# Kernel optimization log

Hardware: AMD Instinct MI355X
Metric: run time of the kernel (lower is better)

The kernel has to match this reference:

```python
import jax, jax.numpy as jnp
import numpy as np

N_HEAD = 16
ROPE_THETA = 10000.0


def _rope_cache(T, dim, theta=ROPE_THETA):
    # inv_freq over even indices, as in RotaryEmbedding
    inv_freq = 1.0 / (theta ** (jnp.arange(0, dim, 2, dtype=jnp.float32) / dim))
    freqs = jnp.arange(T, dtype=jnp.float32)[:, None] * inv_freq[None, :]  # [T, dim//2]
    return jnp.cos(freqs), jnp.sin(freqs)


def _apply_rope(x, cos, sin):
    # x: [B, H, T, D]; cos/sin: [T, D//2] broadcast over B,H
    x1 = x[..., ::2]
    x2 = x[..., 1::2]
    # even slots: x1*cos - x2*sin ; odd slots: x2*cos + x1*sin (interleaved rotate-pairs)
    r1 = x1 * cos - x2 * sin
    r2 = x2 * cos + x1 * sin
    return jnp.stack([r1, r2], axis=-1).reshape(x.shape)


def setup_inputs() -> dict:
    key = jax.random.key(0)
    k1, k2, k3 = jax.random.split(key, 3)
    B, T, C = 4, 2048, 1024
    x = jax.random.normal(k1, (B, T, C), dtype=jnp.float32)
    W_qkv = jax.random.normal(k2, (C, 3 * C), dtype=jnp.float32) * (C ** -0.5)
    W_out = jax.random.normal(k3, (C, C), dtype=jnp.float32) * (C ** -0.5)
    return {"x": x, "W_qkv": W_qkv, "W_out": W_out}


def reference(x, W_qkv, W_out):
    B, T, C = x.shape
    H = N_HEAD
    D = C // H
    # fused QKV projection -> [3, B, H, T, D]
    qkv = (x @ W_qkv).reshape(B, T, 3, H, D).transpose(2, 0, 3, 1, 4)
    q, k, v = qkv[0], qkv[1], qkv[2]
    cos, sin = _rope_cache(T, D)
    q = _apply_rope(q, cos, sin)
    k = _apply_rope(k, cos, sin)
    scale = 1.0 / jnp.sqrt(jnp.float32(D))
    scores = jnp.einsum('bhqd,bhkd->bhqk', q, k) * scale  # [B,H,T,T]
    causal_mask = jnp.tril(jnp.ones((T, T), dtype=bool))
    scores = jnp.where(causal_mask, scores, -jnp.inf)
    attn = jax.nn.softmax(scores, axis=-1)
    out = jnp.einsum('bhqk,bhkd->bhqd', attn, v)  # [B,H,T,D]
    out = out.transpose(0, 2, 1, 3).reshape(B, T, C)
    return out @ W_out
```

## Files before the change

kernel.cpp:

```cpp
#include <hip/hip_runtime.h>
#include <hip/hip_bf16.h>
#include <math.h>

#define BATCH 4
#define SEQ   2048
#define CDIM  1024
#define NHEAD 16
#define HDIM  64
#define QKVN  3072
#define QSCALE 0.1803368801111244f

typedef float f32x4 __attribute__((ext_vector_type(4)));
typedef short bf16x8 __attribute__((ext_vector_type(8)));
typedef short bf16x4 __attribute__((ext_vector_type(4)));

static __device__ __forceinline__ unsigned short f2bf(float f) {
    unsigned int u = __float_as_uint(f);
    u += 0x7FFF + ((u >> 16) & 1);
    return (unsigned short)(u >> 16);
}
static __device__ __forceinline__ float bf2f(unsigned short u) {
    return __uint_as_float(((unsigned int)u) << 16);
}
static __device__ __forceinline__ unsigned int pk2bf(float lo, float hi) {
    __hip_bfloat162 h = __float22bfloat162_rn(make_float2(lo, hi));
    return *(unsigned int*)&h;
}
static __device__ __forceinline__ bf16x8 lds_read8(const unsigned short* p) {
    bf16x4 lo = *(const bf16x4*)p;
    bf16x4 hi = *(const bf16x4*)(p + 4);
    return __builtin_shufflevector(lo, hi, 0, 1, 2, 3, 4, 5, 6, 7);
}

__global__ __launch_bounds__(256) void convert_bf16(const float* __restrict__ src,
                                                    unsigned short* __restrict__ dst,
                                                    int n4) {
    int i = blockIdx.x * 256 + threadIdx.x;
    if (i >= n4) return;
    float4 v = ((const float4*)src)[i];
    ushort4 o;
    o.x = f2bf(v.x); o.y = f2bf(v.y); o.z = f2bf(v.z); o.w = f2bf(v.w);
    ((ushort4*)dst)[i] = o;
}

__global__ __launch_bounds__(256) void transpose_bf16(const float* __restrict__ W,
                                                      unsigned short* __restrict__ Wt,
                                                      int K, int N) {
    __shared__ unsigned short tile[64][65];
    const int tid = threadIdx.x;
    const int n0 = blockIdx.x * 64;
    const int k0 = blockIdx.y * 64;
    const int r = tid >> 4;
    const int c4 = (tid & 15) << 2;
    #pragma unroll
    for (int ii = 0; ii < 4; ii++) {
        int row = r + 16 * ii;
        float4 v = *(const float4*)&W[(size_t)(k0 + row) * N + n0 + c4];
        tile[c4 + 0][row] = f2bf(v.x);
        tile[c4 + 1][row] = f2bf(v.y);
        tile[c4 + 2][row] = f2bf(v.z);
        tile[c4 + 3][row] = f2bf(v.w);
    }
    __syncthreads();
    #pragma unroll
    for (int ii = 0; ii < 4; ii++) {
        int row = r + 16 * ii;
        ushort4 o;
        o.x = tile[row][c4 + 0];
        o.y = tile[row][c4 + 1];
        o.z = tile[row][c4 + 2];
        o.w = tile[row][c4 + 3];
        *(ushort4*)&Wt[(size_t)(n0 + row) * K + k0 + c4] = o;
    }
}

#define GLDS(gp, lp) __builtin_amdgcn_global_load_lds(                       \
    (const __attribute__((address_space(1))) unsigned int*)(gp),             \
    (__attribute__((address_space(3))) unsigned int*)(lp), 16, 0, 0)

template <typename OUT>
__global__ __launch_bounds__(256) void gemm_bt_bf16(
    const unsigned short* __restrict__ A,
    const unsigned short* __restrict__ Bt,
    OUT* __restrict__ C, int M, int N, int K) {
    __shared__ unsigned short As[128 * 32];
    __shared__ unsigned short Bs[128 * 32];

    const int tid = threadIdx.x;
    const int wave = tid >> 6;
    const int lane = tid & 63;
    const int bm = blockIdx.y * 128;
    const int bn = blockIdx.x * 128;
    const int wm = (wave >> 1) * 64;
    const int wn = (wave & 1) * 64;

    const int srow = tid >> 2;
    const int scol = (((tid & 3) ^ ((tid >> 3) & 3)) << 3);
    const unsigned short* Ag0 = A + (size_t)(bm + srow) * K + scol;
    const unsigned short* Ag1 = A + (size_t)(bm + 64 + srow) * K + scol;
    const unsigned short* Bg0 = Bt + (size_t)(bn + srow) * K + scol;
    const unsigned short* Bg1 = Bt + (size_t)(bn + 64 + srow) * K + scol;
    char* AsW = (char*)As + wave * 1024;
    char* BsW = (char*)Bs + wave * 1024;

    const int fm = lane & 15;
    const int quad = lane >> 4;
    const int ck = (quad ^ ((fm >> 1) & 3)) << 3;

    f32x4 acc[4][4];
    #pragma unroll
    for (int i = 0; i < 4; i++)
        #pragma unroll
        for (int j = 0; j < 4; j++)
            acc[i][j] = (f32x4){0.f, 0.f, 0.f, 0.f};

    for (int k0 = 0; k0 < K; k0 += 32) {
        GLDS(Ag0 + k0, AsW);
        GLDS(Ag1 + k0, AsW + 4096);
        GLDS(Bg0 + k0, BsW);
        GLDS(Bg1 + k0, BsW + 4096);
        __syncthreads();

        bf16x8 af[4], bfr[4];
        #pragma unroll
        for (int i = 0; i < 4; i++)
            af[i] = *(const bf16x8*)&As[(wm + i * 16 + fm) * 32 + ck];
        #pragma unroll
        for (int j = 0; j < 4; j++)
            bfr[j] = *(const bf16x8*)&Bs[(wn + j * 16 + fm) * 32 + ck];
        #pragma unroll
        for (int i = 0; i < 4; i++)
            #pragma unroll
            for (int j = 0; j < 4; j++)
                acc[i][j] = __builtin_amdgcn_mfma_f32_16x16x32_bf16(
                    af[i], bfr[j], acc[i][j], 0, 0, 0);
        __syncthreads();
    }

    const int er = quad * 4;
    #pragma unroll
    for (int i = 0; i < 4; i++) {
        #pragma unroll
        for (int j = 0; j < 4; j++) {
            #pragma unroll
            for (int r = 0; r < 4; r++) {
                size_t off = (size_t)(bm + wm + i * 16 + er + r) * N + bn + wn + j * 16 + fm;
                if constexpr (sizeof(OUT) == 2)
                    C[off] = f2bf(acc[i][j][r]);
                else
                    C[off] = acc[i][j][r];
            }
        }
    }
}

__global__ __launch_bounds__(256) void rope_qk(const unsigned short* __restrict__ qkvb,
                                               unsigned short* __restrict__ Qg,
                                               unsigned short* __restrict__ Kg) {
    const int i = blockIdx.x * 256 + threadIdx.x;
    const int c4 = (i & 15) << 2;
    const int h = (i >> 4) & 15;
    const int s = (i >> 8) & 1;
    const int t = (i >> 9) & 2047;
    const int b = i >> 20;

    ushort4 v = *(const ushort4*)&qkvb[(((size_t)(b * SEQ + t) * 3 + s) * CDIM) + h * HDIM + c4];
    float x0 = bf2f(v.x), x1 = bf2f(v.y), x2 = bf2f(v.z), x3 = bf2f(v.w);
    const float invf0 = powf(10000.0f, -((float)c4) / 64.0f);
    const float invf1 = powf(10000.0f, -((float)(c4 + 2)) / 64.0f);
    float s0, c0, s1, c1;
    __sincosf((float)t * invf0, &s0, &c0);
    __sincosf((float)t * invf1, &s1, &c1);
    const float sc = s == 0 ? QSCALE : 1.0f;
    ushort4 o;
    o.x = f2bf((x0 * c0 - x1 * s0) * sc);
    o.y = f2bf((x1 * c0 + x0 * s0) * sc);
    o.z = f2bf((x2 * c1 - x3 * s1) * sc);
    o.w = f2bf((x3 * c1 + x2 * s1) * sc);
    unsigned short* dst = (s == 0) ? Qg : Kg;
    *(ushort4*)&dst[((size_t)(b * NHEAD + h) * SEQ + t) * HDIM + c4] = o;
}

__global__ __launch_bounds__(256) void transpose_v(const unsigned short* __restrict__ qkvb,
                                                   unsigned short* __restrict__ Vtg) {
    __shared__ unsigned short tile[64 * 68];
    const int tid = threadIdx.x;
    const int tt = blockIdx.x;
    const int bh = blockIdx.y;
    const int b = bh >> 4, h = bh & 15;
    const int r = tid >> 4;
    const int c4 = (tid & 15) << 2;
    #pragma unroll
    for (int ii = 0; ii < 4; ii++) {
        int row = r + 16 * ii;
        ushort4 v = *(const ushort4*)&qkvb[(((size_t)(b * SEQ + tt * 64 + row) * 3 + 2) * CDIM) + h * HDIM + c4];
        *(ushort4*)&tile[row * 68 + c4] = v;
    }
    __syncthreads();
    #pragma unroll
    for (int ii = 0; ii < 4; ii++) {
        int d = r + 16 * ii;
        ushort4 o;
        o.x = tile[(c4 + 0) * 68 + d];
        o.y = tile[(c4 + 1) * 68 + d];
        o.z = tile[(c4 + 2) * 68 + d];
        o.w = tile[(c4 + 3) * 68 + d];
        *(ushort4*)&Vtg[((size_t)bh * HDIM + d) * SEQ + tt * 64 + c4] = o;
    }
}

__global__ __launch_bounds__(256, 4) void flash_attn_mfma(
    const unsigned short* __restrict__ Qg,
    const unsigned short* __restrict__ Kg,
    const unsigned short* __restrict__ Vtg,
    unsigned short* __restrict__ att) {
    __shared__ unsigned short Ks[64 * 68];
    __shared__ unsigned short Vt[64 * 68];
    __shared__ unsigned short Ps[128 * 68];

    const int tid = threadIdx.x;
    const int wave = tid >> 6;
    const int lane = tid & 63;
    const int fm = lane & 15;
    const int quad = lane >> 4;
    const int fq = quad << 3;
    const int wq = wave * 32;
    const int bh = blockIdx.x & 63;
    const int qt = 15 - (blockIdx.x >> 6);
    const int b = bh >> 4, h = bh & 15;

    const int r_ld = tid >> 4;
    const int c4 = (tid & 15) << 2;

    bf16x8 aq[2][2];
    #pragma unroll
    for (int i = 0; i < 2; i++)
        #pragma unroll
        for (int ks = 0; ks < 2; ks++)
            aq[i][ks] = *(const bf16x8*)&Qg[((size_t)bh * SEQ + qt * 128 + wq + i * 16 + fm) * HDIM + ks * 32 + fq];

    bf16x8 bones;
    #pragma unroll
    for (int z = 0; z < 8; z++) bones[z] = (short)0x3F80;

    f32x4 O[2][4], lsum[2];
    #pragma unroll
    for (int i = 0; i < 2; i++) {
        lsum[i] = (f32x4){0.f, 0.f, 0.f, 0.f};
        #pragma unroll
        for (int dt = 0; dt < 4; dt++) O[i][dt] = (f32x4){0.f, 0.f, 0.f, 0.f};
    }

    const int jtop = 2 * qt + 1;
    for (int j = 0; j <= jtop; j++) {
        #pragma unroll
        for (int ii = 0; ii < 4; ii++) {
            const int row = r_ld + 16 * ii;
            *(ushort4*)&Ks[row * 68 + c4] =
                *(const ushort4*)&Kg[((size_t)bh * SEQ + j * 64 + row) * HDIM + c4];
            *(ushort4*)&Vt[row * 68 + c4] =
                *(const ushort4*)&Vtg[((size_t)bh * HDIM + row) * SEQ + j * 64 + c4];
        }
        __syncthreads();

        const bool active = (j * 64) <= (qt * 128 + wq + 31);
        if (active) {
            f32x4 sa[2][4];
            #pragma unroll
            for (int i = 0; i < 2; i++)
                #pragma unroll
                for (int jj = 0; jj < 4; jj++)
                    sa[i][jj] = (f32x4){0.f, 0.f, 0.f, 0.f};
            #pragma unroll
            for (int ks = 0; ks < 2; ks++) {
                #pragma unroll
                for (int jj = 0; jj < 4; jj++) {
                    bf16x8 bk = lds_read8(&Ks[(jj * 16 + fm) * 68 + ks * 32 + fq]);
                    sa[0][jj] = __builtin_amdgcn_mfma_f32_16x16x32_bf16(aq[0][ks], bk, sa[0][jj], 0, 0, 0);
                    sa[1][jj] = __builtin_amdgcn_mfma_f32_16x16x32_bf16(aq[1][ks], bk, sa[1][jj], 0, 0, 0);
                }
            }

            if (j * 64 + 63 > qt * 128 + wq) {
                const int kb = j * 64 + fm;
                #pragma unroll
                for (int i = 0; i < 2; i++) {
                    const int rb = qt * 128 + wq + i * 16 + quad * 4;
                    #pragma unroll
                    for (int jj = 0; jj < 4; jj++)
                        #pragma unroll
                        for (int r = 0; r < 4; r++)
                            if (kb + jj * 16 > rb + r) sa[i][jj][r] = -INFINITY;
                }
            }

            #pragma unroll
            for (int i = 0; i < 2; i++) {
                const int prow = (wq + i * 16 + quad * 4) * 68 + fm;
                #pragma unroll
                for (int jj = 0; jj < 4; jj++) {
                    const float e0 = exp2f(sa[i][jj][0]);
                    const float e1 = exp2f(sa[i][jj][1]);
                    const float e2 = exp2f(sa[i][jj][2]);
                    const float e3 = exp2f(sa[i][jj][3]);
                    const unsigned int p01 = pk2bf(e0, e1);
                    const unsigned int p23 = pk2bf(e2, e3);
                    Ps[prow + 0 * 68 + jj * 16] = (unsigned short)p01;
                    Ps[prow + 1 * 68 + jj * 16] = (unsigned short)(p01 >> 16);
                    Ps[prow + 2 * 68 + jj * 16] = (unsigned short)p23;
                    Ps[prow + 3 * 68 + jj * 16] = (unsigned short)(p23 >> 16);
                }
            }

            #pragma unroll
            for (int ks = 0; ks < 2; ks++) {
                bf16x8 ap0 = lds_read8(&Ps[(wq + fm) * 68 + ks * 32 + fq]);
                bf16x8 ap1 = lds_read8(&Ps[(wq + 16 + fm) * 68 + ks * 32 + fq]);
                lsum[0] = __builtin_amdgcn_mfma_f32_16x16x32_bf16(ap0, bones, lsum[0], 0, 0, 0);
                lsum[1] = __builtin_amdgcn_mfma_f32_16x16x32_bf16(ap1, bones, lsum[1], 0, 0, 0);
                #pragma unroll
                for (int dt = 0; dt < 4; dt++) {
                    bf16x8 bv = lds_read8(&Vt[(dt * 16 + fm) * 68 + ks * 32 + fq]);
                    O[0][dt] = __builtin_amdgcn_mfma_f32_16x16x32_bf16(ap0, bv, O[0][dt], 0, 0, 0);
                    O[1][dt] = __builtin_amdgcn_mfma_f32_16x16x32_bf16(ap1, bv, O[1][dt], 0, 0, 0);
                }
            }
        }
        __syncthreads();
    }

    #pragma unroll
    for (int i = 0; i < 2; i++) {
        #pragma unroll
        for (int r = 0; r < 4; r++) {
            const float inv_l = 1.0f / lsum[i][r];
            const int row = qt * 128 + wq + i * 16 + quad * 4 + r;
            #pragma unroll
            for (int dt = 0; dt < 4; dt++)
                att[(size_t)(b * SEQ + row) * CDIM + h * HDIM + dt * 16 + fm] =
                    f2bf(O[i][dt][r] * inv_l);
        }
    }
}

extern "C" void kernel_launch(void* const* d_in, const int* in_sizes, int n_in,
                              void* d_out, int out_size, void* d_ws, size_t ws_size,
                              hipStream_t stream) {
    const float* x     = (const float*)d_in[0];
    const float* W_qkv = (const float*)d_in[1];
    const float* W_out = (const float*)d_in[2];
    float* out = (float*)d_out;

    const int M = BATCH * SEQ;

    unsigned short* qkvb = (unsigned short*)d_ws;
    unsigned short* xb   = qkvb + (size_t)M * QKVN;
    unsigned short* wqb  = xb + (size_t)M * CDIM;
    unsigned short* wob  = wqb + (size_t)CDIM * QKVN;
    unsigned short* attb = wob + (size_t)CDIM * CDIM;
    unsigned short* Qg   = attb + (size_t)M * CDIM;
    unsigned short* Kg   = Qg + (size_t)M * CDIM;
    unsigned short* Vtg  = Kg + (size_t)M * CDIM;

    convert_bf16<<<(M * CDIM / 4 + 255) / 256, 256, 0, stream>>>(x, xb, M * CDIM / 4);
    transpose_bf16<<<dim3(QKVN / 64, CDIM / 64), 256, 0, stream>>>(W_qkv, wqb, CDIM, QKVN);
    transpose_bf16<<<dim3(CDIM / 64, CDIM / 64), 256, 0, stream>>>(W_out, wob, CDIM, CDIM);

    gemm_bt_bf16<unsigned short><<<dim3(QKVN / 128, M / 128), 256, 0, stream>>>(
        xb, wqb, qkvb, M, QKVN, CDIM);

    rope_qk<<<(BATCH * SEQ * 2 * NHEAD * 16) / 256, 256, 0, stream>>>(qkvb, Qg, Kg);
    transpose_v<<<dim3(SEQ / 64, BATCH * NHEAD), 256, 0, stream>>>(qkvb, Vtg);

    flash_attn_mfma<<<BATCH * NHEAD * (SEQ / 128), 256, 0, stream>>>(Qg, Kg, Vtg, attb);

    gemm_bt_bf16<float><<<dim3(CDIM / 128, M / 128), 256, 0, stream>>>(
        attb, wob, out, M, CDIM, CDIM);
}
```

Baseline: 305.0 us.

## Shrink flash-attention query tile to 64 rows and raise occupancy

The attention kernel now handles 64 query rows per block, with each wave owning 16 rows instead of 32. This doubles the grid, drops the per-wave active-mask branch because the diagonal block is always the last one, halves the P scratch tile and register use, and raises the launch-bounds occupancy hint from 4 to 6. The aim is finer causal load balancing and more blocks resident per CU. The cost is that each K/V tile loaded to shared memory now serves half as many query rows, so global/LDS traffic per unit of work rises.

```diff
diff --git a/kernel.cpp b/kernel.cpp
--- a/kernel.cpp
+++ b/kernel.cpp
@@ -209,14 +209,14 @@
     }
 }
 
-__global__ __launch_bounds__(256, 4) void flash_attn_mfma(
+__global__ __launch_bounds__(256, 6) void flash_attn_mfma(
     const unsigned short* __restrict__ Qg,
     const unsigned short* __restrict__ Kg,
     const unsigned short* __restrict__ Vtg,
     unsigned short* __restrict__ att) {
     __shared__ unsigned short Ks[64 * 68];
     __shared__ unsigned short Vt[64 * 68];
-    __shared__ unsigned short Ps[128 * 68];
+    __shared__ unsigned short Ps[64 * 68];
 
     const int tid = threadIdx.x;
     const int wave = tid >> 6;
@@ -224,35 +224,29 @@
     const int fm = lane & 15;
     const int quad = lane >> 4;
     const int fq = quad << 3;
-    const int wq = wave * 32;
+    const int wq = wave * 16;
     const int bh = blockIdx.x & 63;
-    const int qt = 15 - (blockIdx.x >> 6);
+    const int qt = 31 - (blockIdx.x >> 6);
     const int b = bh >> 4, h = bh & 15;
 
     const int r_ld = tid >> 4;
     const int c4 = (tid & 15) << 2;
 
-    bf16x8 aq[2][2];
-    #pragma unroll
-    for (int i = 0; i < 2; i++)
-        #pragma unroll
-        for (int ks = 0; ks < 2; ks++)
-            aq[i][ks] = *(const bf16x8*)&Qg[((size_t)bh * SEQ + qt * 128 + wq + i * 16 + fm) * HDIM + ks * 32 + fq];
+    bf16x8 aq[2];
+    #pragma unroll
+    for (int ks = 0; ks < 2; ks++)
+        aq[ks] = *(const bf16x8*)&Qg[((size_t)bh * SEQ + qt * 64 + wq + fm) * HDIM + ks * 32 + fq];
 
     bf16x8 bones;
     #pragma unroll
     for (int z = 0; z < 8; z++) bones[z] = (short)0x3F80;
 
-    f32x4 O[2][4], lsum[2];
-    #pragma unroll
-    for (int i = 0; i < 2; i++) {
-        lsum[i] = (f32x4){0.f, 0.f, 0.f, 0.f};
-        #pragma unroll
-        for (int dt = 0; dt < 4; dt++) O[i][dt] = (f32x4){0.f, 0.f, 0.f, 0.f};
-    }
-
-    const int jtop = 2 * qt + 1;
-    for (int j = 0; j <= jtop; j++) {
+    f32x4 O[4], lsum;
+    lsum = (f32x4){0.f, 0.f, 0.f, 0.f};
+    #pragma unroll
+    for (int dt = 0; dt < 4; dt++) O[dt] = (f32x4){0.f, 0.f, 0.f, 0.f};
+
+    for (int j = 0; j <= qt; j++) {
         #pragma unroll
         for (int ii = 0; ii < 4; ii++) {
             const int row = r_ld + 16 * ii;
@@ -263,83 +257,67 @@
         }
         __syncthreads();
 
-        const bool active = (j * 64) <= (qt * 128 + wq + 31);
-        if (active) {
-            f32x4 sa[2][4];
-            #pragma unroll
-            for (int i = 0; i < 2; i++)
+        f32x4 sa[4];
+        #pragma unroll
+        for (int jj = 0; jj < 4; jj++)
+            sa[jj] = (f32x4){0.f, 0.f, 0.f, 0.f};
+        #pragma unroll
+        for (int ks = 0; ks < 2; ks++) {
+            #pragma unroll
+            for (int jj = 0; jj < 4; jj++) {
+                bf16x8 bk = lds_read8(&Ks[(jj * 16 + fm) * 68 + ks * 32 + fq]);
+                sa[jj] = __builtin_amdgcn_mfma_f32_16x16x32_bf16(aq[ks], bk, sa[jj], 0, 0, 0);
+            }
+        }
+
+        if (j == qt) {
+            const int kb = j * 64 + fm;
+            const int rb = qt * 64 + wq + quad * 4;
+            #pragma unroll
+            for (int jj = 0; jj < 4; jj++)
                 #pragma unroll
-                for (int jj = 0; jj < 4; jj++)
-                    sa[i][jj] = (f32x4){0.f, 0.f, 0.f, 0.f};
-            #pragma unroll
-            for (int ks = 0; ks < 2; ks++) {
-                #pragma unroll
-                for (int jj = 0; jj < 4; jj++) {
-                    bf16x8 bk = lds_read8(&Ks[(jj * 16 + fm) * 68 + ks * 32 + fq]);
-                    sa[0][jj] = __builtin_amdgcn_mfma_f32_16x16x32_bf16(aq[0][ks], bk, sa[0][jj], 0, 0, 0);
-                    sa[1][jj] = __builtin_amdgcn_mfma_f32_16x16x32_bf16(aq[1][ks], bk, sa[1][jj], 0, 0, 0);
-                }
+                for (int r = 0; r < 4; r++)
+                    if (kb + jj * 16 > rb + r) sa[jj][r] = -INFINITY;
+        }
+
+        {
+            const int prow = (wq + quad * 4) * 68 + fm;
+            #pragma unroll
+            for (int jj = 0; jj < 4; jj++) {
+                const float e0 = exp2f(sa[jj][0]);
+                const float e1 = exp2f(sa[jj][1]);
+                const float e2 = exp2f(sa[jj][2]);
+                const float e3 = exp2f(sa[jj][3]);
+                const unsigned int p01 = pk2bf(e0, e1);
+                const unsigned int p23 = pk2bf(e2, e3);
+                Ps[prow + 0 * 68 + jj * 16] = (unsigned short)p01;
+                Ps[prow + 1 * 68 + jj * 16] = (unsigned short)(p01 >> 16);
+                Ps[prow + 2 * 68 + jj * 16] = (unsigned short)p23;
+                Ps[prow + 3 * 68 + jj * 16] = (unsigned short)(p23 >> 16);
             }
-
-            if (j * 64 + 63 > qt * 128 + wq) {
-                const int kb = j * 64 + fm;
-                #pragma unroll
-                for (int i = 0; i < 2; i++) {
-                    const int rb = qt * 128 + wq + i * 16 + quad * 4;
-                    #pragma unroll
-                    for (int jj = 0; jj < 4; jj++)
-                        #pragma unroll
-                        for (int r = 0; r < 4; r++)
-                            if (kb + jj * 16 > rb + r) sa[i][jj][r] = -INFINITY;
-                }
+        }
+
+        #pragma unroll
+        for (int ks = 0; ks < 2; ks++) {
+            bf16x8 ap = lds_read8(&Ps[(wq + fm) * 68 + ks * 32 + fq]);
+            lsum = __builtin_amdgcn_mfma_f32_16x16x32_bf16(ap, bones, lsum, 0, 0, 0);
+            #pragma unroll
+            for (int dt = 0; dt < 4; dt++) {
+                bf16x8 bv = lds_read8(&Vt[(dt * 16 + fm) * 68 + ks * 32 + fq]);
+                O[dt] = __builtin_amdgcn_mfma_f32_16x16x32_bf16(ap, bv, O[dt], 0, 0, 0);
             }
-
-            #pragma unroll
-            for (int i = 0; i < 2; i++) {
-                const int prow = (wq + i * 16 + quad * 4) * 68 + fm;
-                #pragma unroll
-                for (int jj = 0; jj < 4; jj++) {
-                    const float e0 = exp2f(sa[i][jj][0]);
-                    const float e1 = exp2f(sa[i][jj][1]);
-                    const float e2 = exp2f(sa[i][jj][2]);
-                    const float e3 = exp2f(sa[i][jj][3]);
-                    const unsigned int p01 = pk2bf(e0, e1);
-                    const unsigned int p23 = pk2bf(e2, e3);
-                    Ps[prow + 0 * 68 + jj * 16] = (unsigned short)p01;
-                    Ps[prow + 1 * 68 + jj * 16] = (unsigned short)(p01 >> 16);
-                    Ps[prow + 2 * 68 + jj * 16] = (unsigned short)p23;
-                    Ps[prow + 3 * 68 + jj * 16] = (unsigned short)(p23 >> 16);
-                }
-            }
-
-            #pragma unroll
-            for (int ks = 0; ks < 2; ks++) {
-                bf16x8 ap0 = lds_read8(&Ps[(wq + fm) * 68 + ks * 32 + fq]);
-                bf16x8 ap1 = lds_read8(&Ps[(wq + 16 + fm) * 68 + ks * 32 + fq]);
-                lsum[0] = __builtin_amdgcn_mfma_f32_16x16x32_bf16(ap0, bones, lsum[0], 0, 0, 0);
-                lsum[1] = __builtin_amdgcn_mfma_f32_16x16x32_bf16(ap1, bones, lsum[1], 0, 0, 0);
-                #pragma unroll
-                for (int dt = 0; dt < 4; dt++) {
-                    bf16x8 bv = lds_read8(&Vt[(dt * 16 + fm) * 68 + ks * 32 + fq]);
-                    O[0][dt] = __builtin_amdgcn_mfma_f32_16x16x32_bf16(ap0, bv, O[0][dt], 0, 0, 0);
-                    O[1][dt] = __builtin_amdgcn_mfma_f32_16x16x32_bf16(ap1, bv, O[1][dt], 0, 0, 0);
-                }
-            }
         }
         __syncthreads();
     }
 
     #pragma unroll
-    for (int i = 0; i < 2; i++) {
-        #pragma unroll
-        for (int r = 0; r < 4; r++) {
-            const float inv_l = 1.0f / lsum[i][r];
-            const int row = qt * 128 + wq + i * 16 + quad * 4 + r;
-            #pragma unroll
-            for (int dt = 0; dt < 4; dt++)
-                att[(size_t)(b * SEQ + row) * CDIM + h * HDIM + dt * 16 + fm] =
-                    f2bf(O[i][dt][r] * inv_l);
-        }
+    for (int r = 0; r < 4; r++) {
+        const float inv_l = 1.0f / lsum[r];
+        const int row = qt * 64 + wq + quad * 4 + r;
+        #pragma unroll
+        for (int dt = 0; dt < 4; dt++)
+            att[(size_t)(b * SEQ + row) * CDIM + h * HDIM + dt * 16 + fm] =
+                f2bf(O[dt][r] * inv_l);
     }
 }
 
@@ -372,7 +350,7 @@
     rope_qk<<<(BATCH * SEQ * 2 * NHEAD * 16) / 256, 256, 0, stream>>>(qkvb, Qg, Kg);
     transpose_v<<<dim3(SEQ / 64, BATCH * NHEAD), 256, 0, stream>>>(qkvb, Vtg);
 
-    flash_attn_mfma<<<BATCH * NHEAD * (SEQ / 128), 256, 0, stream>>>(Qg, Kg, Vtg, attb);
+    flash_attn_mfma<<<BATCH * NHEAD * (SEQ / 64), 256, 0, stream>>>(Qg, Kg, Vtg, attb);
 
     gemm_bt_bf16<float><<<dim3(CDIM / 128, M / 128), 256, 0, stream>>>(
         attb, wob, out, M, CDIM, CDIM);
```

Result: slower. 336.3 us (+10.3%).

## Pair causal query tiles per block and double-buffer K/V loads in attention

Applied to the files above, without the earlier changes.

Each attention block now handles two query tiles (s and 15-s) one after the other, which balances causal work across 512 blocks instead of 1024 blocks of uneven length. K/V tiles are double-buffered in LDS, and the next tile is prefetched into registers while the current one is computed, so there is one barrier per iteration. The cost is more LDS per block and more registers, and launch bounds drop to 2 blocks per CU, which lowers occupancy.

```diff
diff --git a/kernel.cpp b/kernel.cpp
--- a/kernel.cpp
+++ b/kernel.cpp
@@ -209,13 +209,13 @@
     }
 }
 
-__global__ __launch_bounds__(256, 4) void flash_attn_mfma(
+__global__ __launch_bounds__(256, 2) void flash_attn_mfma(
     const unsigned short* __restrict__ Qg,
     const unsigned short* __restrict__ Kg,
     const unsigned short* __restrict__ Vtg,
     unsigned short* __restrict__ att) {
-    __shared__ unsigned short Ks[64 * 68];
-    __shared__ unsigned short Vt[64 * 68];
+    __shared__ unsigned short Ks[2][64 * 68];
+    __shared__ unsigned short Vt[2][64 * 68];
     __shared__ unsigned short Ps[128 * 68];
 
     const int tid = threadIdx.x;
@@ -225,120 +225,161 @@
     const int quad = lane >> 4;
     const int fq = quad << 3;
     const int wq = wave * 32;
-    const int bh = blockIdx.x & 63;
-    const int qt = 15 - (blockIdx.x >> 6);
+    const int blk = blockIdx.x;
+    const int bh = blk & 63;
+    const int p = blk >> 6;
     const int b = bh >> 4, h = bh & 15;
 
     const int r_ld = tid >> 4;
     const int c4 = (tid & 15) << 2;
 
-    bf16x8 aq[2][2];
-    #pragma unroll
-    for (int i = 0; i < 2; i++)
-        #pragma unroll
-        for (int ks = 0; ks < 2; ks++)
-            aq[i][ks] = *(const bf16x8*)&Qg[((size_t)bh * SEQ + qt * 128 + wq + i * 16 + fm) * HDIM + ks * 32 + fq];
-
     bf16x8 bones;
     #pragma unroll
     for (int z = 0; z < 8; z++) bones[z] = (short)0x3F80;
 
-    f32x4 O[2][4], lsum[2];
-    #pragma unroll
-    for (int i = 0; i < 2; i++) {
-        lsum[i] = (f32x4){0.f, 0.f, 0.f, 0.f};
-        #pragma unroll
-        for (int dt = 0; dt < 4; dt++) O[i][dt] = (f32x4){0.f, 0.f, 0.f, 0.f};
-    }
-
-    const int jtop = 2 * qt + 1;
-    for (int j = 0; j <= jtop; j++) {
+    const unsigned short* Kbase = Kg + (size_t)bh * SEQ * HDIM;
+    const unsigned short* Vbase = Vtg + (size_t)bh * HDIM * SEQ;
+
+    #pragma unroll 1
+    for (int ph = 0; ph < 2; ph++) {
+        const int s = ph ? (15 - p) : p;
+
+        bf16x8 aq[2][2];
+        #pragma unroll
+        for (int i = 0; i < 2; i++)
+            #pragma unroll
+            for (int ks = 0; ks < 2; ks++)
+                aq[i][ks] = *(const bf16x8*)&Qg[((size_t)bh * SEQ + s * 128 + wq + i * 16 + fm) * HDIM + ks * 32 + fq];
+
+        f32x4 O[2][4], lsum[2];
+        #pragma unroll
+        for (int i = 0; i < 2; i++) {
+            lsum[i] = (f32x4){0.f, 0.f, 0.f, 0.f};
+            #pragma unroll
+            for (int dt = 0; dt < 4; dt++) O[i][dt] = (f32x4){0.f, 0.f, 0.f, 0.f};
+        }
+
+        const int jmax = 2 * s + 1;
+
+        ushort4 kreg[4], vreg[4];
         #pragma unroll
         for (int ii = 0; ii < 4; ii++) {
             const int row = r_ld + 16 * ii;
-            *(ushort4*)&Ks[row * 68 + c4] =
-                *(const ushort4*)&Kg[((size_t)bh * SEQ + j * 64 + row) * HDIM + c4];
-            *(ushort4*)&Vt[row * 68 + c4] =
-                *(const ushort4*)&Vtg[((size_t)bh * HDIM + row) * SEQ + j * 64 + c4];
+            kreg[ii] = *(const ushort4*)&Kbase[(size_t)row * HDIM + c4];
+            vreg[ii] = *(const ushort4*)&Vbase[(size_t)row * SEQ + c4];
+        }
+        #pragma unroll
+        for (int ii = 0; ii < 4; ii++) {
+            const int row = r_ld + 16 * ii;
+            *(ushort4*)&Ks[0][row * 68 + c4] = kreg[ii];
+            *(ushort4*)&Vt[0][row * 68 + c4] = vreg[ii];
         }
         __syncthreads();
 
-        const bool active = (j * 64) <= (qt * 128 + wq + 31);
-        if (active) {
-            f32x4 sa[2][4];
-            #pragma unroll
-            for (int i = 0; i < 2; i++)
-                #pragma unroll
-                for (int jj = 0; jj < 4; jj++)
-                    sa[i][jj] = (f32x4){0.f, 0.f, 0.f, 0.f};
-            #pragma unroll
-            for (int ks = 0; ks < 2; ks++) {
-                #pragma unroll
-                for (int jj = 0; jj < 4; jj++) {
-                    bf16x8 bk = lds_read8(&Ks[(jj * 16 + fm) * 68 + ks * 32 + fq]);
-                    sa[0][jj] = __builtin_amdgcn_mfma_f32_16x16x32_bf16(aq[0][ks], bk, sa[0][jj], 0, 0, 0);
-                    sa[1][jj] = __builtin_amdgcn_mfma_f32_16x16x32_bf16(aq[1][ks], bk, sa[1][jj], 0, 0, 0);
+        int cur = 0;
+        #pragma unroll 1
+        for (int j = 0; j <= jmax; j++) {
+            if (j < jmax) {
+                #pragma unroll
+                for (int ii = 0; ii < 4; ii++) {
+                    const int row = r_ld + 16 * ii;
+                    kreg[ii] = *(const ushort4*)&Kbase[(size_t)((j + 1) * 64 + row) * HDIM + c4];
+                    vreg[ii] = *(const ushort4*)&Vbase[(size_t)row * SEQ + (j + 1) * 64 + c4];
                 }
             }
 
-            if (j * 64 + 63 > qt * 128 + wq) {
-                const int kb = j * 64 + fm;
-                #pragma unroll
-                for (int i = 0; i < 2; i++) {
-                    const int rb = qt * 128 + wq + i * 16 + quad * 4;
+            const bool active = (j * 64) <= (s * 128 + wq + 31);
+            if (active) {
+                const unsigned short* Kc = Ks[cur];
+                const unsigned short* Vc = Vt[cur];
+
+                f32x4 sa[2][4];
+                #pragma unroll
+                for (int i = 0; i < 2; i++)
                     #pragma unroll
                     for (int jj = 0; jj < 4; jj++)
+                        sa[i][jj] = (f32x4){0.f, 0.f, 0.f, 0.f};
+                #pragma unroll
+                for (int ks = 0; ks < 2; ks++) {
+                    #pragma unroll
+                    for (int jj = 0; jj < 4; jj++) {
+                        bf16x8 bk = lds_read8(&Kc[(jj * 16 + fm) * 68 + ks * 32 + fq]);
+                        sa[0][jj] = __builtin_amdgcn_mfma_f32_16x16x32_bf16(aq[0][ks], bk, sa[0][jj], 0, 0, 0);
+                        sa[1][jj] = __builtin_amdgcn_mfma_f32_16x16x32_bf16(aq[1][ks], bk, sa[1][jj], 0, 0, 0);
+                    }
+                }
+
+                if (j * 64 + 63 > s * 128 + wq) {
+                    const int kb = j * 64 + fm;
+                    #pragma unroll
+                    for (int i = 0; i < 2; i++) {
+                        const int rb = s * 128 + wq + i * 16 + quad * 4;
                         #pragma unroll
-                        for (int r = 0; r < 4; r++)
-                            if (kb + jj * 16 > rb + r) sa[i][jj][r] = -INFINITY;
+                        for (int jj = 0; jj < 4; jj++)
+                            #pragma unroll
+                            for (int r = 0; r < 4; r++)
+                                if (kb + jj * 16 > rb + r) sa[i][jj][r] = -INFINITY;
+                    }
+                }
+
+                #pragma unroll
+                for (int i = 0; i < 2; i++) {
+                    const int prow = (wq + i * 16 + quad * 4) * 68 + fm;
+                    #pragma unroll
+                    for (int jj = 0; jj < 4; jj++) {
+                        const float e0 = exp2f(sa[i][jj][0]);
+                        const float e1 = exp2f(sa[i][jj][1]);
+                        const float e2 = exp2f(sa[i][jj][2]);
+                        const float e3 = exp2f(sa[i][jj][3]);
+                        const unsigned int p01 = pk2bf(e0, e1);
+                        const unsigned int p23 = pk2bf(e2, e3);
+                        Ps[prow + 0 * 68 + jj * 16] = (unsigned short)p01;
+                        Ps[prow + 1 * 68 + jj * 16] = (unsigned short)(p01 >> 16);
+                        Ps[prow + 2 * 68 + jj * 16] = (unsigned short)p23;
+                        Ps[prow + 3 * 68 + jj * 16] = (unsigned short)(p23 >> 16);
+                    }
+                }
+
+                #pragma unroll
+                for (int ks = 0; ks < 2; ks++) {
+                    bf16x8 ap0 = lds_read8(&Ps[(wq + fm) * 68 + ks * 32 + fq]);
+                    bf16x8 ap1 = lds_read8(&Ps[(wq + 16 + fm) * 68 + ks * 32 + fq]);
+                    lsum[0] = __builtin_amdgcn_mfma_f32_16x16x32_bf16(ap0, bones, lsum[0], 0, 0, 0);
+                    lsum[1] = __builtin_amdgcn_mfma_f32_16x16x32_bf16(ap1, bones, lsum[1], 0, 0, 0);
+                    #pragma unroll
+                    for (int dt = 0; dt < 4; dt++) {
+                        bf16x8 bv = lds_read8(&Vc[(dt * 16 + fm) * 68 + ks * 32 + fq]);
+                        O[0][dt] = __builtin_amdgcn_mfma_f32_16x16x32_bf16(ap0, bv, O[0][dt], 0, 0, 0);
+                        O[1][dt] = __builtin_amdgcn_mfma_f32_16x16x32_bf16(ap1, bv, O[1][dt], 0, 0, 0);
+                    }
                 }
             }
 
+            if (j < jmax) {
+                const int nb = cur ^ 1;
+                #pragma unroll
+                for (int ii = 0; ii < 4; ii++) {
+                    const int row = r_ld + 16 * ii;
+                    *(ushort4*)&Ks[nb][row * 68 + c4] = kreg[ii];
+                    *(ushort4*)&Vt[nb][row * 68 + c4] = vreg[ii];
+                }
+            }
+
+            __syncthreads();
+            cur ^= 1;
+        }
+
+        #pragma unroll
+        for (int i = 0; i < 2; i++) {
             #pragma unroll
-            for (int i = 0; i < 2; i++) {
-                const int prow = (wq + i * 16 + quad * 4) * 68 + fm;
-                #pragma unroll
-                for (int jj = 0; jj < 4; jj++) {
-                    const float e0 = exp2f(sa[i][jj][0]);
-                    const float e1 = exp2f(sa[i][jj][1]);
-                    const float e2 = exp2f(sa[i][jj][2]);
-                    const float e3 = exp2f(sa[i][jj][3]);
-                    const unsigned int p01 = pk2bf(e0, e1);
-                    const unsigned int p23 = pk2bf(e2, e3);
-                    Ps[prow + 0 * 68 + jj * 16] = (unsigned short)p01;
-                    Ps[prow + 1 * 68 + jj * 16] = (unsigned short)(p01 >> 16);
-                    Ps[prow + 2 * 68 + jj * 16] = (unsigned short)p23;
-                    Ps[prow + 3 * 68 + jj * 16] = (unsigned short)(p23 >> 16);
-                }
+            for (int r = 0; r < 4; r++) {
+                const float inv_l = 1.0f / lsum[i][r];
+                const int row = s * 128 + wq + i * 16 + quad * 4 + r;
+                #pragma unroll
+                for (int dt = 0; dt < 4; dt++)
+                    att[(size_t)(b * SEQ + row) * CDIM + h * HDIM + dt * 16 + fm] =
+                        f2bf(O[i][dt][r] * inv_l);
             }
-
-            #pragma unroll
-            for (int ks = 0; ks < 2; ks++) {
-                bf16x8 ap0 = lds_read8(&Ps[(wq + fm) * 68 + ks * 32 + fq]);
-                bf16x8 ap1 = lds_read8(&Ps[(wq + 16 + fm) * 68 + ks * 32 + fq]);
-                lsum[0] = __builtin_amdgcn_mfma_f32_16x16x32_bf16(ap0, bones, lsum[0], 0, 0, 0);
-                lsum[1] = __builtin_amdgcn_mfma_f32_16x16x32_bf16(ap1, bones, lsum[1], 0, 0, 0);
-                #pragma unroll
-                for (int dt = 0; dt < 4; dt++) {
-                    bf16x8 bv = lds_read8(&Vt[(dt * 16 + fm) * 68 + ks * 32 + fq]);
-                    O[0][dt] = __builtin_amdgcn_mfma_f32_16x16x32_bf16(ap0, bv, O[0][dt], 0, 0, 0);
-                    O[1][dt] = __builtin_amdgcn_mfma_f32_16x16x32_bf16(ap1, bv, O[1][dt], 0, 0, 0);
-                }
-            }
-        }
-        __syncthreads();
-    }
-
-    #pragma unroll
-    for (int i = 0; i < 2; i++) {
-        #pragma unroll
-        for (int r = 0; r < 4; r++) {
-            const float inv_l = 1.0f / lsum[i][r];
-            const int row = qt * 128 + wq + i * 16 + quad * 4 + r;
-            #pragma unroll
-            for (int dt = 0; dt < 4; dt++)
-                att[(size_t)(b * SEQ + row) * CDIM + h * HDIM + dt * 16 + fm] =
-                    f2bf(O[i][dt][r] * inv_l);
         }
     }
 }
@@ -372,7 +413,7 @@
     rope_qk<<<(BATCH * SEQ * 2 * NHEAD * 16) / 256, 256, 0, stream>>>(qkvb, Qg, Kg);
     transpose_v<<<dim3(SEQ / 64, BATCH * NHEAD), 256, 0, stream>>>(qkvb, Vtg);
 
-    flash_attn_mfma<<<BATCH * NHEAD * (SEQ / 128), 256, 0, stream>>>(Qg, Kg, Vtg, attb);
+    flash_attn_mfma<<<512, 256, 0, stream>>>(Qg, Kg, Vtg, attb);
 
     gemm_bt_bf16<float><<<dim3(CDIM / 128, M / 128), 256, 0, stream>>>(
         attb, wob, out, M, CDIM, CDIM);
```

New measurement: 312.6 us. 2.5% more time.

## Prefetch next K/V tile into registers during attention compute, add MFMA priority

Applied to the files above, without the earlier changes.

The attention loop now issues global loads for the next K and V tiles into registers before computing on the current tile. After a barrier it writes them into shared memory, so global memory latency overlaps with the MFMA and softmax work. It also raises wave priority around the MFMA blocks with s_setprio. The cost is extra register pressure from the staged tiles, plus a second barrier per iteration.

```diff
diff --git a/kernel.cpp b/kernel.cpp
--- a/kernel.cpp
+++ b/kernel.cpp
@@ -232,6 +232,9 @@
     const int r_ld = tid >> 4;
     const int c4 = (tid & 15) << 2;
 
+    const unsigned short* Kbase = Kg + (size_t)bh * SEQ * HDIM;
+    const unsigned short* Vbase = Vtg + (size_t)bh * HDIM * SEQ;
+
     bf16x8 aq[2][2];
     #pragma unroll
     for (int i = 0; i < 2; i++)
@@ -252,16 +255,26 @@
     }
 
     const int jtop = 2 * qt + 1;
+
+    #pragma unroll
+    for (int ii = 0; ii < 4; ii++) {
+        const int row = r_ld + 16 * ii;
+        *(ushort4*)&Ks[row * 68 + c4] = *(const ushort4*)&Kbase[(size_t)row * HDIM + c4];
+        *(ushort4*)&Vt[row * 68 + c4] = *(const ushort4*)&Vbase[(size_t)row * SEQ + c4];
+    }
+    __syncthreads();
+
+    #pragma unroll 1
     for (int j = 0; j <= jtop; j++) {
-        #pragma unroll
-        for (int ii = 0; ii < 4; ii++) {
-            const int row = r_ld + 16 * ii;
-            *(ushort4*)&Ks[row * 68 + c4] =
-                *(const ushort4*)&Kg[((size_t)bh * SEQ + j * 64 + row) * HDIM + c4];
-            *(ushort4*)&Vt[row * 68 + c4] =
-                *(const ushort4*)&Vtg[((size_t)bh * HDIM + row) * SEQ + j * 64 + c4];
+        ushort4 kreg[4], vreg[4];
+        if (j < jtop) {
+            #pragma unroll
+            for (int ii = 0; ii < 4; ii++) {
+                const int row = r_ld + 16 * ii;
+                kreg[ii] = *(const ushort4*)&Kbase[(size_t)((j + 1) * 64 + row) * HDIM + c4];
+                vreg[ii] = *(const ushort4*)&Vbase[(size_t)row * SEQ + (j + 1) * 64 + c4];
+            }
         }
-        __syncthreads();
 
         const bool active = (j * 64) <= (qt * 128 + wq + 31);
         if (active) {
@@ -271,6 +284,7 @@
                 #pragma unroll
                 for (int jj = 0; jj < 4; jj++)
                     sa[i][jj] = (f32x4){0.f, 0.f, 0.f, 0.f};
+            __builtin_amdgcn_s_setprio(1);
             #pragma unroll
             for (int ks = 0; ks < 2; ks++) {
                 #pragma unroll
@@ -280,6 +294,7 @@
                     sa[1][jj] = __builtin_amdgcn_mfma_f32_16x16x32_bf16(aq[1][ks], bk, sa[1][jj], 0, 0, 0);
                 }
             }
+            __builtin_amdgcn_s_setprio(0);
 
             if (j * 64 + 63 > qt * 128 + wq) {
                 const int kb = j * 64 + fm;
@@ -312,6 +327,7 @@
                 }
             }
 
+            __builtin_amdgcn_s_setprio(1);
             #pragma unroll
             for (int ks = 0; ks < 2; ks++) {
                 bf16x8 ap0 = lds_read8(&Ps[(wq + fm) * 68 + ks * 32 + fq]);
@@ -325,6 +341,17 @@
                     O[1][dt] = __builtin_amdgcn_mfma_f32_16x16x32_bf16(ap1, bv, O[1][dt], 0, 0, 0);
                 }
             }
+            __builtin_amdgcn_s_setprio(0);
+        }
+
+        __syncthreads();
+        if (j < jtop) {
+            #pragma unroll
+            for (int ii = 0; ii < 4; ii++) {
+                const int row = r_ld + 16 * ii;
+                *(ushort4*)&Ks[row * 68 + c4] = kreg[ii];
+                *(ushort4*)&Vt[row * 68 + c4] = vreg[ii];
+            }
         }
         __syncthreads();
     }
```

New measurement: 338.6 us. 1.11x slower.
